# Optimization experiments

Hardware: AMD Instinct MI355X
Metric: run time of the kernel (lower is better)

Reference implementation:

```python
import jax, jax.numpy as jnp
import numpy as np

B, L, D, F, K, M = 32, 1024, 384, 384, 3, 4096
LN_EPS = 1e-5


def setup_inputs() -> dict:
    key = jax.random.key(0)
    ks = jax.random.split(key, 6)
    w = lambda k, shp: jax.random.normal(k, shp, jnp.float32) * 0.02
    return {
        "x": jax.random.normal(ks[0], (B, L, D), jnp.float32),
        "target": jax.random.randint(ks[1], (B, L), 0, 5),
        "mel_max_length": M,
        "conv1_w": w(ks[2], (F, D, K)),  # OIW layout
        "conv1_b": jnp.zeros((F,), jnp.float32),
        "ln1_g": jnp.ones((F,), jnp.float32),
        "ln1_b": jnp.zeros((F,), jnp.float32),
        "conv2_w": w(ks[3], (F, F, K)),
        "conv2_b": jnp.zeros((F,), jnp.float32),
        "ln2_g": jnp.ones((F,), jnp.float32),
        "ln2_b": jnp.zeros((F,), jnp.float32),
        "lin_w": w(ks[4], (F, 1)),
        "lin_b": jnp.zeros((1,), jnp.float32),
    }


def conv1d_same(x, w, b):
    # x: [B, L, C], w: [O, I, K] -> [B, L, O], 'same' padding
    pad = (w.shape[-1] - 1) // 2
    y = jax.lax.conv_general_dilated(
        x, w, window_strides=(1,), padding=[(pad, pad)],
        dimension_numbers=("NWC", "OIW", "NWC"))
    return y + b


def layernorm(x, g, b):
    m = jnp.mean(x, axis=-1, keepdims=True)
    v = jnp.mean(jnp.square(x - m), axis=-1, keepdims=True)
    return (x - m) * jax.lax.rsqrt(v + LN_EPS) * g + b


def duration_predictor(x, c1w, c1b, g1, b1, c2w, c2b, g2, b2, lw, lb):
    h = jnp.maximum(layernorm(conv1d_same(x, c1w, c1b), g1, b1), 0.0)
    h = jnp.maximum(layernorm(conv1d_same(h, c2w, c2b), g2, b2), 0.0)
    return jnp.maximum(h @ lw + lb, 0.0)[..., 0]  # [B, L]


def length_regulate(x, durations, mel_max_length):
    # Equivalent to one-hot alignment matmul + zero pad, done as a gather.
    cum = jnp.cumsum(durations, axis=1)  # [B, L]
    t = jnp.arange(mel_max_length)       # [M]
    # frame t belongs to phoneme j where cum[j-1] <= t < cum[j]
    idx = jax.vmap(lambda c: jnp.searchsorted(c, t, side="right"))(cum)  # [B, M]
    valid = (t[None, :] < cum[:, -1:]).astype(x.dtype)                    # [B, M]
    idx = jnp.minimum(idx, durations.shape[1] - 1)
    out = jnp.take_along_axis(x, idx[..., None], axis=1) * valid[..., None]
    return out  # [B, M, D]


def reference(x, target, mel_max_length, conv1_w, conv1_b, ln1_g, ln1_b,
              conv2_w, conv2_b, ln2_g, ln2_b, lin_w, lin_b):
    dur_pred = duration_predictor(x, conv1_w, conv1_b, ln1_g, ln1_b,
                                  conv2_w, conv2_b, ln2_g, ln2_b, lin_w, lin_b)
    out = length_regulate(x, target, mel_max_length)
    return out, dur_pred
```

## Files before the change

### kernel.cpp

```cpp
#include <hip/hip_runtime.h>

#define DEV __device__ __forceinline__

typedef unsigned short u16;
typedef __attribute__((ext_vector_type(8))) short bf16x8;
typedef __attribute__((ext_vector_type(8))) unsigned short u16x8;
typedef __attribute__((ext_vector_type(4))) float f32x4;

constexpr int Bz = 32, Lz = 1024, Dz = 384, Fz = 384, KWz = 3, Mz = 4096;
constexpr float EPS = 1e-5f;

DEV u16 f2bf(float f) {
  unsigned u = __float_as_uint(f);
  u += 0x7fffu + ((u >> 16) & 1u);
  return (u16)(u >> 16);
}

typedef __attribute__((address_space(1))) const unsigned char ga_t;
typedef __attribute__((address_space(3))) unsigned char la_t;
DEV void gload16(const void* g, void* l) {
  __builtin_amdgcn_global_load_lds((ga_t*)g, (la_t*)l, 16, 0, 0);
}

#define WAITV(n) asm volatile("s_waitcnt vmcnt(" #n ")" ::: "memory")

__global__ __launch_bounds__(1024) void k_pre(
    const float* __restrict__ w1, const float* __restrict__ w2,
    u16* __restrict__ w1t, u16* __restrict__ w2t, u16* __restrict__ h1,
    const int* __restrict__ tgt, int* __restrict__ idxb) {
  __shared__ int sc[Lz];
  constexpr int WT = KWz * Fz * Dz;
  constexpr int PREP_ELEMS = 2 * WT + Bz * 2 * Dz;
  constexpr int PREP_BLKS = (PREP_ELEMS + 1023) / 1024;
  const int tid = threadIdx.x;

  if (blockIdx.x < PREP_BLKS) {
    int gid = blockIdx.x * 1024 + tid;
    if (gid < WT) {
      int k = gid / (Fz * Dz), rem = gid % (Fz * Dz);
      int f = rem / Dz, d = rem % Dz;
      w1t[gid] = f2bf(w1[(f * Dz + d) * KWz + k]);
    } else if (gid < 2 * WT) {
      int g2 = gid - WT;
      int k = g2 / (Fz * Fz), rem = g2 % (Fz * Fz);
      int co = rem / Fz, ci = rem % Fz;
      w2t[g2] = f2bf(w2[(co * Fz + ci) * KWz + k]);
    } else if (gid < PREP_ELEMS) {
      int p = gid - 2 * WT;
      int b = p / (2 * Dz), r = (p / Dz) & 1, d = p % Dz;
      size_t row = (size_t)b * (Lz + 2) + (r ? (Lz + 1) : 0);
      h1[row * Dz + d] = 0;
    }
    return;
  }
  int b = blockIdx.x - PREP_BLKS;
  sc[tid] = tgt[b * Lz + tid];
  __syncthreads();
  for (int off = 1; off < Lz; off <<= 1) {
    int add = (tid >= off) ? sc[tid - off] : 0;
    __syncthreads();
    sc[tid] += add;
    __syncthreads();
  }
  int total = sc[Lz - 1];
  for (int t = tid; t < Mz; t += 1024) {
    int lo = 0, hi = Lz;
    while (lo < hi) {
      int mid = (lo + hi) >> 1;
      if (sc[mid] > t) hi = mid; else lo = mid + 1;
    }
    int iv = (t < total) ? (lo > Lz - 1 ? Lz - 1 : lo) : -1;
    idxb[b * Mz + t] = iv;
  }
}

__global__ void k_gather(const float* __restrict__ x, const int* __restrict__ idxb,
                         float* __restrict__ out) {
  int wid = (blockIdx.x * blockDim.x + threadIdx.x) >> 6;
  int lane = threadIdx.x & 63;
  int nw = (gridDim.x * blockDim.x) >> 6;
  for (int row = wid; row < Bz * Mz; row += nw) {
    int b = row >> 12;
    int iv = idxb[row];
    f32x4* dst = reinterpret_cast<f32x4*>(out + (size_t)row * Dz);
    if (iv < 0) {
      f32x4 z = {0.f, 0.f, 0.f, 0.f};
      __builtin_nontemporal_store(z, dst + lane);
      if (lane < 32) __builtin_nontemporal_store(z, dst + 64 + lane);
    } else {
      const f32x4* src =
          reinterpret_cast<const f32x4*>(x + ((size_t)b * Lz + iv) * Dz);
      f32x4 a = src[lane];
      __builtin_nontemporal_store(a, dst + lane);
      if (lane < 32) {
        f32x4 c = src[64 + lane];
        __builtin_nontemporal_store(c, dst + 64 + lane);
      }
    }
  }
}

template <int LAYER>
__global__ __launch_bounds__(512, 2) void k_conv(
    const void* __restrict__ Asrc,
    const u16* __restrict__ wt,
    const float* __restrict__ cbias,
    const float* __restrict__ lng, const float* __restrict__ lnb,
    u16* __restrict__ hout,
    const float* __restrict__ lw, const float* __restrict__ lbias,
    float* __restrict__ dur)
{
  constexpr int ABUFS = (LAYER == 1) ? 2 : 3;
  __shared__ __align__(16) u16 Ash[ABUFS][8192];
  __shared__ __align__(16) u16 Bsh[3][384 * 32];
  __shared__ float s_sum[4][128], s_sq[4][128], s_dot[4][128];

  const int tid = threadIdx.x;
  const int lane = tid & 63, wave = tid >> 6;
  const int wr = wave >> 2, wc = wave & 3;
  const int l15 = lane & 15, lh = lane >> 4;
  const int b = blockIdx.x >> 3, l0 = (blockIdx.x & 7) << 7;
  const bf16x8 zfrag = {0, 0, 0, 0, 0, 0, 0, 0};

  int bgof[3], bldo[3];
  #pragma unroll
  for (int i = 0; i < 3; ++i) {
    int c = wave + 8 * i;
    int slot = c * 64 + lane, f = slot >> 2, q = slot & 3;
    int ks = q ^ ((f >> 1) & 3);
    bgof[i] = f * 384 + ks * 8;
    bldo[i] = c * 512;
  }
  auto STAGE_B = [&](int kt) {
    int tap = kt % 3, dw = kt / 3;
    const u16* sb = wt + tap * (384 * 384) + dw * 32;
    u16* dst = Bsh[tap];
    #pragma unroll
    for (int i = 0; i < 3; ++i) gload16(sb + bgof[i], dst + bldo[i]);
  };

  const float* arow_ptr = nullptr;
  const u16* a2src[2] = {nullptr, nullptr};
  int a2ldo[2] = {0, 0};
  float4 ar0, ar1, ar2, ar3;
  if constexpr (LAYER == 1) {
    int r1 = tid & 255, g1 = tid >> 8;
    int grow = l0 - 1 + r1;
    if (grow > l0 + 135) grow = l0 + 135;
    if (grow < 0) grow = 0;
    if (grow > Lz - 1) grow = Lz - 1;
    arow_ptr = (const float*)Asrc + (size_t)b * Lz * 384 + (size_t)grow * 384 +
               g1 * 8;
  } else {
    #pragma unroll
    for (int i = 0; i < 2; ++i) {
      int c = wave + 8 * i;
      int s = c * 64 + lane, g = s >> 8, r = s & 255;
      int p = l0 + r;
      if (p > l0 + 135) p = l0 + 135;
      if (p > Lz + 1) p = Lz + 1;
      a2src[i] = (const u16*)Asrc + (size_t)b * (Lz + 2) * 384 +
                 (size_t)p * 384 + g * 8;
      a2ldo[i] = c * 512;
    }
  }
  auto AISSUE = [&](int w) {
    const float* p = arow_ptr + w * 32;
    ar0 = *reinterpret_cast<const float4*>(p);
    ar1 = *reinterpret_cast<const float4*>(p + 4);
    ar2 = *reinterpret_cast<const float4*>(p + 16);
    ar3 = *reinterpret_cast<const float4*>(p + 20);
  };
  auto ADSW = [&](int wbuf) {
    u16x8 h0, h1;
    h0[0] = f2bf(ar0.x); h0[1] = f2bf(ar0.y); h0[2] = f2bf(ar0.z); h0[3] = f2bf(ar0.w);
    h0[4] = f2bf(ar1.x); h0[5] = f2bf(ar1.y); h0[6] = f2bf(ar1.z); h0[7] = f2bf(ar1.w);
    h1[0] = f2bf(ar2.x); h1[1] = f2bf(ar2.y); h1[2] = f2bf(ar2.z); h1[3] = f2bf(ar2.w);
    h1[4] = f2bf(ar3.x); h1[5] = f2bf(ar3.y); h1[6] = f2bf(ar3.z); h1[7] = f2bf(ar3.w);
    *reinterpret_cast<u16x8*>(&Ash[wbuf][tid * 8]) = h0;
    *reinterpret_cast<u16x8*>(&Ash[wbuf][(tid + 512) * 8]) = h1;
  };
  auto STAGE_A2 = [&](int w, int buf) {
    #pragma unroll
    for (int i = 0; i < 2; ++i) gload16(a2src[i] + w * 32, &Ash[buf][a2ldo[i]]);
  };

  int tr[4], boff[6];
  #pragma unroll
  for (int m = 0; m < 4; ++m) tr[m] = wr * 64 + m * 16 + l15;
  #pragma unroll
  for (int n = 0; n < 6; ++n) {
    int c = wc * 96 + n * 16 + l15;
    boff[n] = c * 32 + (lh ^ ((c >> 1) & 3)) * 8;
  }

  f32x4 acc[4][6] = {};

  if constexpr (LAYER == 1) {
    AISSUE(0);
    WAITV(0);
    ADSW(0);
    AISSUE(1);
    __builtin_amdgcn_sched_barrier(0);
    STAGE_B(0);
    STAGE_B(1);
  } else {
    STAGE_A2(0, 0);
    STAGE_B(0);
    STAGE_A2(1, 1);
    STAGE_B(1);
  }

#define PHASE(T)                                                               \
  {                                                                            \
    if constexpr ((T) == 0) {                                                  \
      if constexpr (LAYER == 2) {                                              \
        if (w == 0) { WAITV(5); } else { WAITV(3); }                           \
      } else { WAITV(3); }                                                     \
    } else if constexpr ((T) == 1) {                                           \
      if (w <= 9) {                                                            \
        if constexpr (LAYER == 1) { WAITV(7); } else { WAITV(5); }             \
      } else { WAITV(3); }                                                     \
    } else {                                                                   \
      if (w <= 9) {                                                            \
        if constexpr (LAYER == 1) { WAITV(7); } else { WAITV(5); }             \
      } else if (w == 10) { WAITV(3); } else { WAITV(0); }                     \
    }                                                                          \
    asm volatile("s_waitcnt lgkmcnt(0)" ::: "memory");                         \
    __builtin_amdgcn_s_barrier();                                              \
    __builtin_amdgcn_sched_barrier(0);                                         \
    const int abuf_ = (LAYER == 1) ? (w & 1) : (w % 3);                        \
    bf16x8 av[4], bv[6];                                                       \
    _Pragma("unroll")                                                          \
    for (int m = 0; m < 4; ++m) {                                              \
      av[m] = *reinterpret_cast<const bf16x8*>(                                \
          &Ash[abuf_][(lh * 256 + tr[m] + (T)) * 8]);                          \
      if constexpr (LAYER == 1 && (T) != 1) {                                  \
        int gr = l0 + tr[m] + (T) - 1;                                         \
        if ((unsigned)gr > (unsigned)(Lz - 1)) av[m] = zfrag;                  \
      }                                                                        \
    }                                                                          \
    _Pragma("unroll")                                                          \
    for (int n = 0; n < 6; ++n)                                                \
      bv[n] = *reinterpret_cast<const bf16x8*>(&Bsh[(T)][boff[n]]);            \
    __builtin_amdgcn_sched_barrier(0);                                         \
    { int kt2_ = 3 * w + (T) + 2; if (kt2_ <= 35) STAGE_B(kt2_); }             \
    __builtin_amdgcn_sched_barrier(0);                                         \
    if constexpr (LAYER == 1 && (T) == 0) {                                    \
      if (w <= 10) ADSW((w + 1) & 1);       \
    }                                                                          \
    if constexpr ((T) == 0) {                                                  \
      if (w <= 9) {                                                            \
        if constexpr (LAYER == 1) { AISSUE(w + 2); }                           \
        else { STAGE_A2(w + 2, (w + 2) % 3); }                                 \
      }                                                                        \
    }                                                                          \
    __builtin_amdgcn_sched_barrier(0);                                         \
    __builtin_amdgcn_s_setprio(1);                                             \
    _Pragma("unroll")                                                          \
    for (int m = 0; m < 4; ++m)                                                \
      _Pragma("unroll")                                                        \
      for (int n = 0; n < 6; ++n)                                              \
        acc[m][n] = __builtin_amdgcn_mfma_f32_16x16x32_bf16(av[m], bv[n],      \
                                                            acc[m][n], 0, 0, 0);\
    __builtin_amdgcn_s_setprio(0);                                             \
  }

  for (int w = 0; w < 12; ++w) {
    PHASE(0)
    PHASE(1)
    PHASE(2)
  }
#undef PHASE

  __syncthreads();
  float gv[6], bvv[6], cbv[6], lwv[6];
  #pragma unroll
  for (int n = 0; n < 6; ++n) {
    int c = wc * 96 + n * 16 + l15;
    gv[n] = lng[c]; bvv[n] = lnb[c]; cbv[n] = cbias[c];
    lwv[n] = (LAYER == 2) ? lw[c] : 0.f;
  }
  #pragma unroll
  for (int m = 0; m < 4; ++m) {
    #pragma unroll
    for (int r = 0; r < 4; ++r) {
      float s = 0.f, q2 = 0.f;
      #pragma unroll
      for (int n = 0; n < 6; ++n) {
        float v = acc[m][n][r] + cbv[n];
        s += v; q2 += v * v;
      }
      #pragma unroll
      for (int off = 1; off < 16; off <<= 1) {
        s += __shfl_xor(s, off);
        q2 += __shfl_xor(q2, off);
      }
      if (l15 == 0) {
        int row = wr * 64 + m * 16 + lh * 4 + r;
        s_sum[wc][row] = s;
        s_sq[wc][row] = q2;
      }
    }
  }
  __syncthreads();
  #pragma unroll
  for (int m = 0; m < 4; ++m) {
    #pragma unroll
    for (int r = 0; r < 4; ++r) {
      int row = wr * 64 + m * 16 + lh * 4 + r;
      float S = 0.f, Q = 0.f;
      #pragma unroll
      for (int w = 0; w < 4; ++w) { S += s_sum[w][row]; Q += s_sq[w][row]; }
      float mean = S * (1.f / 384.f);
      float var = Q * (1.f / 384.f) - mean * mean;
      float rstd = rsqrtf(var + EPS);
      float dotp = 0.f;
      #pragma unroll
      for (int n = 0; n < 6; ++n) {
        float v = acc[m][n][r] + cbv[n];
        float y = fmaxf((v - mean) * rstd * gv[n] + bvv[n], 0.f);
        if constexpr (LAYER == 1) {
          int c = wc * 96 + n * 16 + l15;
          hout[((size_t)(b * (Lz + 2) + l0 + row + 1)) * 384 + c] = f2bf(y);
        } else {
          dotp += y * lwv[n];
        }
      }
      if constexpr (LAYER == 2) {
        #pragma unroll
        for (int off = 1; off < 16; off <<= 1) dotp += __shfl_xor(dotp, off);
        if (l15 == 0) s_dot[wc][row] = dotp;
      }
    }
  }
  if constexpr (LAYER == 2) {
    __syncthreads();
    if (tid < 128) {
      float dsum = lbias[0];
      #pragma unroll
      for (int w = 0; w < 4; ++w) dsum += s_dot[w][tid];
      dur[(size_t)b * Lz + l0 + tid] = fmaxf(dsum, 0.f);
    }
  }
}

extern "C" void kernel_launch(void* const* d_in, const int* in_sizes, int n_in,
                              void* d_out, int out_size, void* d_ws, size_t ws_size,
                              hipStream_t stream) {
  (void)in_sizes; (void)n_in; (void)out_size; (void)ws_size;
  const float* x   = (const float*)d_in[0];
  const int* tgt   = (const int*)d_in[1];
  const float* w1  = (const float*)d_in[3];
  const float* c1b = (const float*)d_in[4];
  const float* g1  = (const float*)d_in[5];
  const float* b1  = (const float*)d_in[6];
  const float* w2  = (const float*)d_in[7];
  const float* c2b = (const float*)d_in[8];
  const float* g2  = (const float*)d_in[9];
  const float* b2  = (const float*)d_in[10];
  const float* lw  = (const float*)d_in[11];
  const float* lb  = (const float*)d_in[12];

  float* out0 = (float*)d_out;
  float* dur  = out0 + (size_t)Bz * Mz * Dz;

  const size_t h1_n = (size_t)Bz * (Lz + 2) * Dz;
  const size_t wt_n = (size_t)KWz * Fz * Dz;
  u16* h1  = (u16*)d_ws;
  u16* w1t = h1 + h1_n;
  u16* w2t = w1t + wt_n;
  int* idxb = (int*)(w2t + wt_n);

  constexpr int PREP_BLKS =
      (2 * KWz * Fz * Dz + Bz * 2 * Dz + 1023) / 1024;
  k_pre<<<PREP_BLKS + Bz, 1024, 0, stream>>>(w1, w2, w1t, w2t, h1, tgt, idxb);
  k_conv<1><<<256, 512, 0, stream>>>(x, w1t, c1b, g1, b1, h1, nullptr, nullptr,
                                     nullptr);
  k_conv<2><<<256, 512, 0, stream>>>(h1, w2t, c2b, g2, b2, nullptr, lw, lb, dur);
  k_gather<<<4096, 256, 0, stream>>>(x, idxb, out0);
}
```

Baseline: 119.5 us.

## Double-buffer fragment registers and deepen B-weight LDS ring to four stages

Restructures the conv GEMM main loop so each phase loads the next k-step's A/B fragments from LDS into a second register set before issuing MFMAs on the current set, overlapping LDS reads with matrix math. The B weight staging ring grows from three to four buffers and prefetches three k-steps ahead instead of two. The loop is unrolled by two to alternate the register sets. This raises register and LDS use, so launch bounds drop to one block per SIMD-pair target, which may lower occupancy.

Result: slower. 137.0 us (+14.7%).

```diff
diff --git a/kernel.cpp b/kernel.cpp
--- a/kernel.cpp
+++ b/kernel.cpp
@@ -101,7 +101,7 @@
 }
 
 template <int LAYER>
-__global__ __launch_bounds__(512, 2) void k_conv(
+__global__ __launch_bounds__(512, 1) void k_conv(
     const void* __restrict__ Asrc,
     const u16* __restrict__ wt,
     const float* __restrict__ cbias,
@@ -112,7 +112,7 @@
 {
   constexpr int ABUFS = (LAYER == 1) ? 2 : 3;
   __shared__ __align__(16) u16 Ash[ABUFS][8192];
-  __shared__ __align__(16) u16 Bsh[3][384 * 32];
+  __shared__ __align__(16) u16 Bsh[4][384 * 32];
   __shared__ float s_sum[4][128], s_sq[4][128], s_dot[4][128];
 
   const int tid = threadIdx.x;
@@ -134,7 +134,7 @@
   auto STAGE_B = [&](int kt) {
     int tap = kt % 3, dw = kt / 3;
     const u16* sb = wt + tap * (384 * 384) + dw * 32;
-    u16* dst = Bsh[tap];
+    u16* dst = Bsh[kt & 3];
     #pragma unroll
     for (int i = 0; i < 3; ++i) gload16(sb + bgof[i], dst + bldo[i]);
   };
@@ -195,6 +195,7 @@
   }
 
   f32x4 acc[4][6] = {};
+  bf16x8 av0[4], bv0[6], av1[4], bv1[6];
 
   if constexpr (LAYER == 1) {
     AISSUE(0);
@@ -204,55 +205,68 @@
     __builtin_amdgcn_sched_barrier(0);
     STAGE_B(0);
     STAGE_B(1);
+    STAGE_B(2);
   } else {
     STAGE_A2(0, 0);
+    STAGE_A2(1, 1);
     STAGE_B(0);
-    STAGE_A2(1, 1);
     STAGE_B(1);
-  }
-
-#define PHASE(T)                                                               \
+    STAGE_B(2);
+  }
+  WAITV(6);
+  asm volatile("s_waitcnt lgkmcnt(0)" ::: "memory");
+  __builtin_amdgcn_s_barrier();
+  __builtin_amdgcn_sched_barrier(0);
+  #pragma unroll
+  for (int m = 0; m < 4; ++m) {
+    av0[m] = *reinterpret_cast<const bf16x8*>(&Ash[0][(lh * 256 + tr[m]) * 8]);
+    if constexpr (LAYER == 1) {
+      int gr = l0 + tr[m] - 1;
+      if ((unsigned)gr > (unsigned)(Lz - 1)) av0[m] = zfrag;
+    }
+  }
+  #pragma unroll
+  for (int n = 0; n < 6; ++n)
+    bv0[n] = *reinterpret_cast<const bf16x8*>(&Bsh[0][boff[n]]);
+
+#define PHASE(W, T, AVC, BVC, AVN, BVN)                                        \
   {                                                                            \
-    if constexpr ((T) == 0) {                                                  \
-      if constexpr (LAYER == 2) {                                              \
-        if (w == 0) { WAITV(5); } else { WAITV(3); }                           \
-      } else { WAITV(3); }                                                     \
-    } else if constexpr ((T) == 1) {                                           \
-      if (w <= 9) {                                                            \
+    if constexpr ((T) == 0) { WAITV(3); }                                      \
+    else {                                                                     \
+      if ((W) <= 9) {                                                          \
         if constexpr (LAYER == 1) { WAITV(7); } else { WAITV(5); }             \
-      } else { WAITV(3); }                                                     \
-    } else {                                                                   \
-      if (w <= 9) {                                                            \
-        if constexpr (LAYER == 1) { WAITV(7); } else { WAITV(5); }             \
-      } else if (w == 10) { WAITV(3); } else { WAITV(0); }                     \
+      } else if ((W) == 10) { WAITV(3); } else { WAITV(0); }                   \
     }                                                                          \
     asm volatile("s_waitcnt lgkmcnt(0)" ::: "memory");                         \
     __builtin_amdgcn_s_barrier();                                              \
     __builtin_amdgcn_sched_barrier(0);                                         \
-    const int abuf_ = (LAYER == 1) ? (w & 1) : (w % 3);                        \
-    bf16x8 av[4], bv[6];                                                       \
-    _Pragma("unroll")                                                          \
-    for (int m = 0; m < 4; ++m) {                                              \
-      av[m] = *reinterpret_cast<const bf16x8*>(                                \
-          &Ash[abuf_][(lh * 256 + tr[m] + (T)) * 8]);                          \
-      if constexpr (LAYER == 1 && (T) != 1) {                                  \
-        int gr = l0 + tr[m] + (T) - 1;                                         \
-        if ((unsigned)gr > (unsigned)(Lz - 1)) av[m] = zfrag;                  \
+                      \
+    if ((T) < 2 || (W) <= 10) {                                                \
+      constexpr int tN = ((T) + 1) % 3;                                        \
+      const int wN = (W) + (((T) == 2) ? 1 : 0);                               \
+      const int ktn = 3 * (W) + (T) + 1;                                       \
+      const int abN = (LAYER == 1) ? (wN & 1) : (wN % 3);                      \
+      _Pragma("unroll")                                                        \
+      for (int m = 0; m < 4; ++m) {                                            \
+        AVN[m] = *reinterpret_cast<const bf16x8*>(                             \
+            &Ash[abN][(lh * 256 + tr[m] + tN) * 8]);                           \
+        if constexpr (LAYER == 1 && tN != 1) {                                 \
+          int gr = l0 + tr[m] + tN - 1;                                        \
+          if ((unsigned)gr > (unsigned)(Lz - 1)) AVN[m] = zfrag;               \
+        }                                                                      \
       }                                                                        \
+      _Pragma("unroll")                                                        \
+      for (int n = 0; n < 6; ++n)                                              \
+        BVN[n] = *reinterpret_cast<const bf16x8*>(&Bsh[ktn & 3][boff[n]]);     \
     }                                                                          \
-    _Pragma("unroll")                                                          \
-    for (int n = 0; n < 6; ++n)                                                \
-      bv[n] = *reinterpret_cast<const bf16x8*>(&Bsh[(T)][boff[n]]);            \
     __builtin_amdgcn_sched_barrier(0);                                         \
-    { int kt2_ = 3 * w + (T) + 2; if (kt2_ <= 35) STAGE_B(kt2_); }             \
-    __builtin_amdgcn_sched_barrier(0);                                         \
-    if constexpr (LAYER == 1 && (T) == 0) {                                    \
-      if (w <= 10) ADSW((w + 1) & 1);       \
-    }                                                                          \
+    if ((W) <= 10) STAGE_B(3 * (W) + (T) + 3);                                 \
     if constexpr ((T) == 0) {                                                  \
-      if (w <= 9) {                                                            \
-        if constexpr (LAYER == 1) { AISSUE(w + 2); }                           \
-        else { STAGE_A2(w + 2, (w + 2) % 3); }                                 \
+      if constexpr (LAYER == 1) {                                              \
+        if ((W) <= 10) ADSW(((W) + 1) & 1);                                    \
+        if ((W) <= 9) AISSUE((W) + 2);                                         \
+      } else {                                                                 \
+        if ((W) <= 9) STAGE_A2((W) + 2, ((W) + 2) % 3);                        \
       }                                                                        \
     }                                                                          \
     __builtin_amdgcn_sched_barrier(0);                                         \
@@ -261,15 +275,19 @@
     for (int m = 0; m < 4; ++m)                                                \
       _Pragma("unroll")                                                        \
       for (int n = 0; n < 6; ++n)                                              \
-        acc[m][n] = __builtin_amdgcn_mfma_f32_16x16x32_bf16(av[m], bv[n],      \
+        acc[m][n] = __builtin_amdgcn_mfma_f32_16x16x32_bf16(AVC[m], BVC[n],    \
                                                             acc[m][n], 0, 0, 0);\
     __builtin_amdgcn_s_setprio(0);                                             \
   }
 
-  for (int w = 0; w < 12; ++w) {
-    PHASE(0)
-    PHASE(1)
-    PHASE(2)
+  for (int w2 = 0; w2 < 6; ++w2) {
+    const int we = 2 * w2, wo = 2 * w2 + 1;
+    PHASE(we, 0, av0, bv0, av1, bv1)
+    PHASE(we, 1, av1, bv1, av0, bv0)
+    PHASE(we, 2, av0, bv0, av1, bv1)
+    PHASE(wo, 0, av1, bv1, av0, bv0)
+    PHASE(wo, 1, av0, bv0, av1, bv1)
+    PHASE(wo, 2, av1, bv1, av0, bv0)
   }
 #undef PHASE
 
```
